# Optimization experiments

Hardware: AMD Instinct MI355X
Metric: run time of the kernel (lower is better)

The kernel has to match this reference:

```python
import jax, jax.numpy as jnp
import numpy as np

VOCAB = 780
HIDDEN = 256
DEPTH = 6
N_NODES = 65536
N_MESS = 131072
MAX_NEI = 5
N_TREES = 2048


def setup_inputs() -> dict:
    key = jax.random.key(0)
    ks = jax.random.split(key, 16)
    s = 0.05  # weight scale to avoid gate saturation
    return {
        "fnode": jax.random.randint(ks[0], (N_NODES,), 0, VOCAB),
        "fmess": jax.random.randint(ks[1], (N_MESS,), 0, N_NODES),
        "node_graph": jax.random.randint(ks[2], (N_NODES, MAX_NEI), 0, N_MESS),
        "mess_graph": jax.random.randint(ks[3], (N_MESS, MAX_NEI), 0, N_MESS),
        "scope_ids": jnp.sort(jax.random.randint(ks[4], (N_NODES,), 0, N_TREES)),
        "emb": jax.random.normal(ks[5], (VOCAB, HIDDEN), jnp.float32) * s,
        "Wz_w": jax.random.normal(ks[6], (2 * HIDDEN, HIDDEN), jnp.float32) * s,
        "Wz_b": jax.random.normal(ks[7], (HIDDEN,), jnp.float32) * s,
        "Wr_w": jax.random.normal(ks[8], (HIDDEN, HIDDEN), jnp.float32) * s,
        "Ur_w": jax.random.normal(ks[9], (HIDDEN, HIDDEN), jnp.float32) * s,
        "Ur_b": jax.random.normal(ks[10], (HIDDEN,), jnp.float32) * s,
        "Wh_w": jax.random.normal(ks[11], (2 * HIDDEN, HIDDEN), jnp.float32) * s,
        "Wh_b": jax.random.normal(ks[12], (HIDDEN,), jnp.float32) * s,
        "out_w": jax.random.normal(ks[13], (2 * HIDDEN, HIDDEN), jnp.float32) * s,
        "out_b": jax.random.normal(ks[14], (HIDDEN,), jnp.float32) * s,
    }


def reference(fnode, fmess, node_graph, mess_graph, scope_ids,
              emb, Wz_w, Wz_b, Wr_w, Ur_w, Ur_b, Wh_w, Wh_b, out_w, out_b):
    x_node = emb[fnode]            # [N, H] embedding lookup
    x = x_node[fmess]              # [M, H] source-node feature per message
    M = mess_graph.shape[0]
    mask = jnp.ones((M, 1), x.dtype).at[0].set(0.0)  # message 0 is padding
    r1 = x @ Wr_w                  # W_r(x), constant across depth (no bias)

    def gru_step(h, _):
        h_nei = h[mess_graph]                                  # [M, K, H] gather
        sum_h = h_nei.sum(axis=1)                              # [M, H]
        z = jax.nn.sigmoid(jnp.concatenate([x, sum_h], 1) @ Wz_w + Wz_b)
        r = jax.nn.sigmoid(r1[:, None, :] + h_nei @ Ur_w + Ur_b)  # [M, K, H]
        sum_gh = (r * h_nei).sum(axis=1)
        pre_h = jnp.tanh(jnp.concatenate([x, sum_gh], 1) @ Wh_w + Wh_b)
        h_new = ((1.0 - z) * sum_h + z * pre_h) * mask
        return h_new, None

    h0 = jnp.zeros((M, HIDDEN), x.dtype)
    h, _ = jax.lax.scan(gru_step, h0, None, length=DEPTH)

    mess_nei = h[node_graph].sum(axis=1)                       # [N, H]
    node_vec = jax.nn.relu(jnp.concatenate([x_node, mess_nei], 1) @ out_w + out_b)

    # per-tree mean over contiguous scopes (segment mean)
    sums = jax.ops.segment_sum(node_vec, scope_ids, num_segments=N_TREES)
    counts = jax.ops.segment_sum(jnp.ones((node_vec.shape[0],), node_vec.dtype),
                                 scope_ids, num_segments=N_TREES)
    return sums / jnp.maximum(counts, 1.0)[:, None]
```

## Files before the change

### kernel.cpp

```cpp
#include <hip/hip_runtime.h>


#define HD 256
#define NNODES 65536
#define NMESS 131072
#define NVOCAB 780
#define NTREES 2048
#define MAXNEI 5
#define BM 128
#define BMF 32
#define LDF 264

typedef short bfrag __attribute__((ext_vector_type(8)));
typedef short s16x8 __attribute__((ext_vector_type(8)));
typedef float f32x4v __attribute__((ext_vector_type(4)));
typedef float f32x2 __attribute__((ext_vector_type(2)));
typedef unsigned short ush;
typedef unsigned char u8;

__device__ __forceinline__ float bf2f(ush u) {
    union { unsigned int u; float f; } v; v.u = ((unsigned int)u) << 16; return v.f;
}
__device__ __forceinline__ float bfu_lo(unsigned int w) {
    union { unsigned int u; float f; } v; v.u = w << 16; return v.f;
}
__device__ __forceinline__ float bfu_hi(unsigned int w) {
    union { unsigned int u; float f; } v; v.u = w & 0xffff0000u; return v.f;
}
__device__ __forceinline__ ush f2bf_fast(float f) {
    union { float f; unsigned int u; } v; v.f = f;
    return (ush)((v.u + 0x8000u) >> 16);
}
__device__ __forceinline__ unsigned int pack2bf(float hi, float lo) {
    union { float f; unsigned int u; } a, b; a.f = hi; b.f = lo;
    return __builtin_amdgcn_perm(a.u + 0x8000u, b.u + 0x8000u, 0x07060302u);
}
__device__ __forceinline__ float sigm(float x) {
    return __builtin_amdgcn_rcpf(1.f + __expf(-x));
}
__device__ __forceinline__ float tanh_fast(float x) {
    return 1.f - 2.f * __builtin_amdgcn_rcpf(__expf(2.f * x) + 1.f);
}
__device__ __forceinline__ void async16(const ush* g, ush* l) {
    __builtin_amdgcn_global_load_lds(
        (const __attribute__((address_space(1))) unsigned int*)(g),
        (__attribute__((address_space(3))) unsigned int*)(l), 16, 0, 0);
}
__device__ __forceinline__ uint2 pack8fp8(const float* f) {
    int lo = __builtin_amdgcn_cvt_pk_fp8_f32(f[0], f[1], 0, 0);
    lo = __builtin_amdgcn_cvt_pk_fp8_f32(f[2], f[3], lo, 1);
    int hi = __builtin_amdgcn_cvt_pk_fp8_f32(f[4], f[5], 0, 0);
    hi = __builtin_amdgcn_cvt_pk_fp8_f32(f[6], f[7], hi, 1);
    uint2 o; o.x = (unsigned int)lo; o.y = (unsigned int)hi; return o;
}

__global__ __launch_bounds__(256) void prep_tables_sk(
    const float* __restrict__ emb,
    const float* __restrict__ Wz_w, const float* __restrict__ Wz_b,
    const float* __restrict__ Wr_w, const float* __restrict__ Ur_b,
    const float* __restrict__ Wh_w, const float* __restrict__ Wh_b,
    const float* __restrict__ out_w, const float* __restrict__ out_b,
    float* __restrict__ embR, float* __restrict__ embZ,
    float* __restrict__ embH, float* __restrict__ embO)
{
    __shared__ __align__(16) float e[4][64];
    int t = threadIdx.x;
    int b0 = blockIdx.x * 4;
    int k0 = blockIdx.y * 64;
    e[t >> 6][t & 63] = emb[(b0 + (t >> 6)) * HD + k0 + (t & 63)];
    __syncthreads();
    float aR[4] = {0,0,0,0}, aZ[4] = {0,0,0,0}, aH[4] = {0,0,0,0}, aO[4] = {0,0,0,0};
    for (int kk = 0; kk < 64; kk++) {
        int k = k0 + kk;
        float wr = Wr_w[k * HD + t];
        float wz = Wz_w[k * HD + t];
        float wh = Wh_w[k * HD + t];
        float wo = out_w[k * HD + t];
        #pragma unroll
        for (int r = 0; r < 4; r++) {
            float ev = e[r][kk];
            aR[r] += ev * wr; aZ[r] += ev * wz; aH[r] += ev * wh; aO[r] += ev * wo;
        }
    }
    if (blockIdx.y == 0) {
        float br = Ur_b[t], bz = Wz_b[t], bh = Wh_b[t], bo = out_b[t];
        #pragma unroll
        for (int r = 0; r < 4; r++) { aR[r] += br; aZ[r] += bz; aH[r] += bh; aO[r] += bo; }
    }
    #pragma unroll
    for (int r = 0; r < 4; r++) {
        atomicAdd(&embR[(b0 + r) * HD + t], aR[r]);
        atomicAdd(&embZ[(b0 + r) * HD + t], aZ[r]);
        atomicAdd(&embH[(b0 + r) * HD + t], aH[r]);
        atomicAdd(&embO[(b0 + r) * HD + t], aO[r]);
    }
}

__global__ __launch_bounds__(256) void h1fill(
    const float* __restrict__ embZ, const float* __restrict__ embH,
    ush* __restrict__ h1tab)
{
    int i = blockIdx.x * HD + threadIdx.x;
    h1tab[i] = f2bf_fast(sigm(embZ[i]) * tanh_fast(embH[i]));
}

__global__ __launch_bounds__(256) void h1u_sk(
    const ush* __restrict__ h1tab, const float* __restrict__ Ur_w,
    float* __restrict__ embU)
{
    __shared__ __align__(16) float e[4][64];
    int t = threadIdx.x;
    int b0 = blockIdx.x * 4;
    int k0 = blockIdx.y * 64;
    e[t >> 6][t & 63] = bf2f(h1tab[(b0 + (t >> 6)) * HD + k0 + (t & 63)]);
    __syncthreads();
    float aU[4] = {0,0,0,0};
    for (int kk = 0; kk < 64; kk++) {
        float w = Ur_w[(k0 + kk) * HD + t];
        #pragma unroll
        for (int r = 0; r < 4; r++) aU[r] += e[r][kk] * w;
    }
    #pragma unroll
    for (int r = 0; r < 4; r++) atomicAdd(&embU[(b0 + r) * HD + t], aU[r]);
}

__global__ __launch_bounds__(256) void prep_wt(
    const float* __restrict__ Ur_w, const float* __restrict__ Wz_w,
    const float* __restrict__ Wh_w, const float* __restrict__ out_w,
    ush* __restrict__ Wo2T,
    ush* __restrict__ Wz_p, ush* __restrict__ Wh_p, ush* __restrict__ Ur_p)
{
    int idx = blockIdx.x * 256 + threadIdx.x;
    int n = idx >> 8, k = idx & 255;
    Wo2T[idx] = f2bf_fast(out_w[(HD + k) * HD + n]);
    int paddr = ((((n >> 4) * 8 + (k >> 5)) * 64 + ((k >> 3) & 3) * 16 + (n & 15)) << 3) + (k & 7);
    Wz_p[paddr] = f2bf_fast(Wz_w[(HD + k) * HD + n]);
    Wh_p[paddr] = f2bf_fast(Wh_w[(HD + k) * HD + n]);
    Ur_p[paddr] = f2bf_fast(Ur_w[k * HD + n]);
}

__global__ __launch_bounds__(256) void prep_vmess(
    const int* __restrict__ fnode, const int* __restrict__ fmess,
    int* __restrict__ v_mess)
{
    int m = blockIdx.x * 256 + threadIdx.x;
    v_mess[m] = fnode[fmess[m]];
}

__global__ __launch_bounds__(256) void fill_h1(
    const ush* __restrict__ h1tab, const float* __restrict__ embU,
    const int* __restrict__ v_mess,
    ush* __restrict__ h, u8* __restrict__ hU8)
{
    int t = blockIdx.x * 256 + threadIdx.x;
    int m = t >> 5;
    int c = (t & 31) * 8;
    int v = v_mess[m];
    s16x8 o = *(const s16x8*)&h1tab[v * HD + c];
    float u[8];
    *(float4*)&u[0] = *(const float4*)&embU[v * HD + c];
    *(float4*)&u[4] = *(const float4*)&embU[v * HD + c + 4];
    uint2 up = pack8fp8(u);
    if (m == 0) { o = (s16x8){0,0,0,0,0,0,0,0}; up.x = up.y = 0; }
    *(s16x8*)&h[(size_t)m * HD + c] = o;
    *(uint2*)&hU8[(size_t)m * HD + c] = up;
}

__global__ __launch_bounds__(512) void gemm_out(
    const ush* __restrict__ A, const ush* __restrict__ Bt,
    float* __restrict__ C,
    const float* __restrict__ etab, const int* __restrict__ vids)
{
    __shared__ __align__(16) ush As[BM * 64];
    __shared__ __align__(16) ush Bs[HD * 64];
    int tid = threadIdx.x;
    int wave = tid >> 6, lane = tid & 63;
    int wm = wave >> 2, wn = wave & 3;
    int quad = lane >> 4, l16 = lane & 15;
    int row0 = blockIdx.x * BM;

    const ush* aG[2]; ush* aL[2];
    const ush* bG[4]; ush* bL[4];
    #pragma unroll
    for (int u = 0; u < 2; u++) {
        int cch = wave * 2 + u;
        int s = cch * 64 + lane;
        int r = s >> 3, p = s & 7, q = p ^ (r & 7);
        aG[u] = A + (size_t)(row0 + r) * HD + q * 8;
        aL[u] = &As[cch * 512];
    }
    #pragma unroll
    for (int u = 0; u < 4; u++) {
        int cch = wave * 4 + u;
        int s = cch * 64 + lane;
        int r = s >> 3, p = s & 7, q = p ^ (r & 7);
        bG[u] = Bt + (size_t)r * HD + q * 8;
        bL[u] = &Bs[cch * 512];
    }

    f32x4v acc[4][4] = {};

    for (int k0 = 0; k0 < HD; k0 += 64) {
        #pragma unroll
        for (int u = 0; u < 2; u++) async16(aG[u] + k0, aL[u]);
        #pragma unroll
        for (int u = 0; u < 4; u++) async16(bG[u] + k0, bL[u]);
        __syncthreads();
        #pragma unroll
        for (int ks = 0; ks < 64; ks += 32) {
            bfrag af[4], bff[4];
            #pragma unroll
            for (int i = 0; i < 4; i++) {
                int r = wm * 64 + i * 16 + l16;
                int q = (ks >> 3) + quad, p = q ^ (r & 7);
                af[i] = *(const bfrag*)&As[r * 64 + p * 8];
            }
            #pragma unroll
            for (int j = 0; j < 4; j++) {
                int r = wn * 64 + j * 16 + l16;
                int q = (ks >> 3) + quad, p = q ^ (r & 7);
                bff[j] = *(const bfrag*)&Bs[r * 64 + p * 8];
            }
            #pragma unroll
            for (int i = 0; i < 4; i++)
                #pragma unroll
                for (int j = 0; j < 4; j++)
                    acc[i][j] = __builtin_amdgcn_mfma_f32_16x16x32_bf16(af[i], bff[j], acc[i][j], 0, 0, 0);
        }
        __syncthreads();
    }
    #pragma unroll
    for (int i = 0; i < 4; i++) {
        #pragma unroll
        for (int j = 0; j < 4; j++) {
            int Cc = wn * 64 + j * 16 + l16;
            #pragma unroll
            for (int r = 0; r < 4; r++) {
                int Rr = row0 + wm * 64 + i * 16 + quad * 4 + r;
                float o = acc[i][j][r] + etab[vids[Rr] * HD + Cc];
                C[(size_t)Rr * HD + Cc] = fmaxf(o, 0.f);
            }
        }
    }
}

template<int EMIT_HU>
__global__ __launch_bounds__(256, 4) void fused_step(
    const ush* __restrict__ h, const u8* __restrict__ hU8,
    const int* __restrict__ mg, const int* __restrict__ v_mess,
    const float* __restrict__ embR, const float* __restrict__ embZ,
    const float* __restrict__ embH,
    const ush* __restrict__ Wz_p, const ush* __restrict__ Wh_p,
    const ush* __restrict__ Ur_p,
    ush* __restrict__ h_next, u8* __restrict__ hU8_next)
{
    __shared__ __align__(16) ush sh[BMF * LDF];
    __shared__ __align__(16) ush sg[BMF * LDF];
    int tid = threadIdx.x;
    int wv = tid >> 6, lane = tid & 63;
    int quad = lane >> 4, l16 = lane & 15;
    int m0 = blockIdx.x * BMF;

    #pragma unroll 2
    for (int it = 0; it < 4; it++) {
        int g = it * 256 + tid;
        int ml = g >> 5;
        int c = (g & 31) * 8;
        int m = m0 + ml;
        int v = v_mess[m];
        float rb[8];
        *(float4*)&rb[0] = *(const float4*)&embR[v * HD + c];
        *(float4*)&rb[4] = *(const float4*)&embR[v * HD + c + 4];
        float ah[8] = {0,0,0,0,0,0,0,0};
        float ag[8] = {0,0,0,0,0,0,0,0};
        #pragma unroll
        for (int kn = 0; kn < MAXNEI; kn++) {
            int j = mg[m * MAXNEI + kn];
            s16x8 hv = *(const s16x8*)&h[(size_t)j * HD + c];
            uint2 uv = *(const uint2*)&hU8[(size_t)j * HD + c];
            f32x2 u01 = __builtin_amdgcn_cvt_pk_f32_fp8((int)uv.x, false);
            f32x2 u23 = __builtin_amdgcn_cvt_pk_f32_fp8((int)uv.x, true);
            f32x2 u45 = __builtin_amdgcn_cvt_pk_f32_fp8((int)uv.y, false);
            f32x2 u67 = __builtin_amdgcn_cvt_pk_f32_fp8((int)uv.y, true);
            float uf[8] = {u01.x, u01.y, u23.x, u23.y, u45.x, u45.y, u67.x, u67.y};
            #pragma unroll
            for (int e = 0; e < 8; e++) {
                float hf = bf2f((ush)hv[e]);
                ah[e] += hf;
                ag[e] += sigm(rb[e] + uf[e]) * hf;
            }
        }
        uint4 oh, og;
        oh.x = pack2bf(ah[1], ah[0]); oh.y = pack2bf(ah[3], ah[2]);
        oh.z = pack2bf(ah[5], ah[4]); oh.w = pack2bf(ah[7], ah[6]);
        og.x = pack2bf(ag[1], ag[0]); og.y = pack2bf(ag[3], ag[2]);
        og.z = pack2bf(ag[5], ag[4]); og.w = pack2bf(ag[7], ag[6]);
        *(uint4*)&sh[ml * LDF + c] = oh;
        *(uint4*)&sg[ml * LDF + c] = og;
    }
    __syncthreads();

    f32x4v az[2][4] = {}, ap[2][4] = {};
    #pragma unroll
    for (int ksi = 0; ksi < 8; ksi++) {
        int ks = ksi * 32;
        bfrag ahf[2], agf[2], bz[4], bh[4];
        #pragma unroll
        for (int i = 0; i < 2; i++) {
            ahf[i] = *(const bfrag*)&sh[(i * 16 + l16) * LDF + ks + quad * 8];
            agf[i] = *(const bfrag*)&sg[(i * 16 + l16) * LDF + ks + quad * 8];
        }
        #pragma unroll
        for (int j = 0; j < 4; j++) {
            int f = ((wv * 4 + j) * 8 + ksi) * 64 + lane;
            bz[j] = *(const bfrag*)&Wz_p[(size_t)f * 8];
            bh[j] = *(const bfrag*)&Wh_p[(size_t)f * 8];
        }
        #pragma unroll
        for (int i = 0; i < 2; i++)
            #pragma unroll
            for (int j = 0; j < 4; j++) {
                az[i][j] = __builtin_amdgcn_mfma_f32_16x16x32_bf16(ahf[i], bz[j], az[i][j], 0, 0, 0);
                ap[i][j] = __builtin_amdgcn_mfma_f32_16x16x32_bf16(agf[i], bh[j], ap[i][j], 0, 0, 0);
            }
    }

    #pragma unroll
    for (int i = 0; i < 2; i++) {
        #pragma unroll
        for (int r = 0; r < 4; r++) {
            int rl = i * 16 + quad * 4 + r;
            int Rg = m0 + rl;
            int v = v_mess[Rg];
            #pragma unroll
            for (int j = 0; j < 4; j++) {
                int col = wv * 64 + j * 16 + l16;
                float z = sigm(az[i][j][r] + embZ[v * HD + col]);
                float pre = tanh_fast(ap[i][j][r] + embH[v * HD + col]);
                float shv = bf2f(sh[rl * LDF + col]);
                float hn = (1.f - z) * shv + z * pre;
                if (Rg == 0) hn = 0.f;
                az[i][j][r] = hn;
            }
        }
    }
    __syncthreads();

    #pragma unroll
    for (int i = 0; i < 2; i++)
        #pragma unroll
        for (int j = 0; j < 4; j++) {
            int col = wv * 64 + j * 16 + l16;
            #pragma unroll
            for (int r = 0; r < 4; r++)
                sg[(i * 16 + quad * 4 + r) * LDF + col] = f2bf_fast(az[i][j][r]);
        }
    __syncthreads();
    #pragma unroll
    for (int it = 0; it < 4; it++) {
        int g = it * 256 + tid;
        int ml = g >> 5;
        int c = (g & 31) * 8;
        *(uint4*)&h_next[(size_t)(m0 + ml) * HD + c] = *(const uint4*)&sg[ml * LDF + c];
    }

    if (EMIT_HU) {
        f32x4v au[2][4] = {};
        #pragma unroll
        for (int ksi = 0; ksi < 8; ksi++) {
            int ks = ksi * 32;
            bfrag af[2], bu[4];
            #pragma unroll
            for (int i = 0; i < 2; i++)
                af[i] = *(const bfrag*)&sg[(i * 16 + l16) * LDF + ks + quad * 8];
            #pragma unroll
            for (int j = 0; j < 4; j++) {
                int f = ((wv * 4 + j) * 8 + ksi) * 64 + lane;
                bu[j] = *(const bfrag*)&Ur_p[(size_t)f * 8];
            }
            #pragma unroll
            for (int i = 0; i < 2; i++)
                #pragma unroll
                for (int j = 0; j < 4; j++)
                    au[i][j] = __builtin_amdgcn_mfma_f32_16x16x32_bf16(af[i], bu[j], au[i][j], 0, 0, 0);
        }
        #pragma unroll
        for (int i = 0; i < 2; i++)
            #pragma unroll
            for (int j = 0; j < 4; j++) {
                int col = wv * 64 + j * 16 + l16;
                #pragma unroll
                for (int r = 0; r < 4; r++)
                    sh[(i * 16 + quad * 4 + r) * LDF + col] = f2bf_fast(au[i][j][r]);
            }
        __syncthreads();
        #pragma unroll
        for (int it = 0; it < 4; it++) {
            int g = it * 256 + tid;
            int ml = g >> 5;
            int c = (g & 31) * 8;
            uint4 w = *(const uint4*)&sh[ml * LDF + c];
            float f[8] = { bfu_lo(w.x), bfu_hi(w.x), bfu_lo(w.y), bfu_hi(w.y),
                           bfu_lo(w.z), bfu_hi(w.z), bfu_lo(w.w), bfu_hi(w.w) };
            uint2 o = pack8fp8(f);
            *(uint2*)&hU8_next[(size_t)(m0 + ml) * HD + c] = o;
        }
    }
}

__global__ __launch_bounds__(256) void gather_nodes(
    const ush* __restrict__ h, const int* __restrict__ ng,
    ush* __restrict__ mess_nei)
{
    int wave = threadIdx.x >> 6, lane = threadIdx.x & 63;
    int half = lane >> 5, li = lane & 31;
    int n = blockIdx.x * 8 + wave * 2 + half;
    int c = li * 8;
    float a[8] = {0,0,0,0,0,0,0,0};
    #pragma unroll
    for (int k = 0; k < MAXNEI; k++) {
        int j = ng[n * MAXNEI + k];
        s16x8 hv = *(const s16x8*)&h[(size_t)j * HD + c];
        #pragma unroll
        for (int e = 0; e < 8; e++) a[e] += bf2f((ush)hv[e]);
    }
    uint4 o;
    o.x = pack2bf(a[1], a[0]); o.y = pack2bf(a[3], a[2]);
    o.z = pack2bf(a[5], a[4]); o.w = pack2bf(a[7], a[6]);
    *(uint4*)&mess_nei[(size_t)n * HD + c] = o;
}

__device__ __forceinline__ int lower_bound_dev(const int* a, int n, int key) {
    int lo = 0, hi = n;
    while (lo < hi) { int mid = (lo + hi) >> 1; if (a[mid] < key) lo = mid + 1; else hi = mid; }
    return lo;
}

__global__ __launch_bounds__(256) void segment_mean(
    const float* __restrict__ node_vec, const int* __restrict__ scope,
    float* __restrict__ out)
{
    int t = blockIdx.x;
    int c = threadIdx.x;
    int lo = lower_bound_dev(scope, NNODES, t);
    int hi = lower_bound_dev(scope, NNODES, t + 1);
    float acc = 0.f;
    for (int n = lo; n < hi; n++) acc += node_vec[(size_t)n * HD + c];
    int cnt = hi - lo;
    out[t * HD + c] = cnt > 0 ? acc / (float)cnt : 0.f;
}

extern "C" void kernel_launch(void* const* d_in, const int* in_sizes, int n_in,
                              void* d_out, int out_size, void* d_ws, size_t ws_size,
                              hipStream_t stream)
{
    const int*   fnode      = (const int*)d_in[0];
    const int*   fmess      = (const int*)d_in[1];
    const int*   node_graph = (const int*)d_in[2];
    const int*   mess_graph = (const int*)d_in[3];
    const int*   scope_ids  = (const int*)d_in[4];
    const float* emb        = (const float*)d_in[5];
    const float* Wz_w       = (const float*)d_in[6];
    const float* Wz_b       = (const float*)d_in[7];
    const float* Wr_w       = (const float*)d_in[8];
    const float* Ur_w       = (const float*)d_in[9];
    const float* Ur_b       = (const float*)d_in[10];
    const float* Wh_w       = (const float*)d_in[11];
    const float* Wh_b       = (const float*)d_in[12];
    const float* out_w      = (const float*)d_in[13];
    const float* out_b      = (const float*)d_in[14];

    char* ws = (char*)d_ws;
    const size_t MHB = (size_t)NMESS * HD * 2;
    const size_t MH8 = (size_t)NMESS * HD;
    ush* P0 = (ush*)ws; ws += MHB;
    ush* P1 = (ush*)ws; ws += MHB;
    u8* U0 = (u8*)ws; ws += MH8;
    u8* U1 = (u8*)ws; ws += MH8;
    float* embR = (float*)ws; ws += (size_t)NVOCAB * HD * 4;
    float* embZ = (float*)ws; ws += (size_t)NVOCAB * HD * 4;
    float* embH = (float*)ws; ws += (size_t)NVOCAB * HD * 4;
    float* embO = (float*)ws; ws += (size_t)NVOCAB * HD * 4;
    float* embU = (float*)ws; ws += (size_t)NVOCAB * HD * 4;
    ush* h1tab = (ush*)ws; ws += (size_t)NVOCAB * HD * 2;
    ush* Wo2T  = (ush*)ws; ws += (size_t)HD * HD * 2;
    ush* Wz_p  = (ush*)ws; ws += (size_t)HD * HD * 2;
    ush* Wh_p  = (ush*)ws; ws += (size_t)HD * HD * 2;
    ush* Ur_p  = (ush*)ws; ws += (size_t)HD * HD * 2;
    int* v_mess = (int*)ws; ws += (size_t)NMESS * 4;
    if ((size_t)(ws - (char*)d_ws) > ws_size) return;

    hipMemsetAsync(embR, 0, (size_t)5 * NVOCAB * HD * 4, stream);
    prep_tables_sk<<<dim3(NVOCAB / 4, 4), 256, 0, stream>>>(
        emb, Wz_w, Wz_b, Wr_w, Ur_b, Wh_w, Wh_b, out_w, out_b,
        embR, embZ, embH, embO);
    h1fill<<<NVOCAB, 256, 0, stream>>>(embZ, embH, h1tab);
    h1u_sk<<<dim3(NVOCAB / 4, 4), 256, 0, stream>>>(h1tab, Ur_w, embU);
    prep_wt<<<HD * HD / 256, 256, 0, stream>>>(Ur_w, Wz_w, Wh_w, out_w,
                                               Wo2T, Wz_p, Wh_p, Ur_p);
    prep_vmess<<<NMESS / 256, 256, 0, stream>>>(fnode, fmess, v_mess);
    fill_h1<<<NMESS * 32 / 256, 256, 0, stream>>>(h1tab, embU, v_mess, P0, U0);

    ush* hc = P0; ush* hn = P1;
    u8* uc = U0; u8* un = U1;
    for (int d = 1; d < 5; d++) {
        fused_step<1><<<NMESS / BMF, 256, 0, stream>>>(hc, uc, mess_graph, v_mess,
                                                       embR, embZ, embH,
                                                       Wz_p, Wh_p, Ur_p, hn, un);
        { ush* t = hc; hc = hn; hn = t; }
        { u8* t = uc; uc = un; un = t; }
    }
    fused_step<0><<<NMESS / BMF, 256, 0, stream>>>(hc, uc, mess_graph, v_mess,
                                                   embR, embZ, embH,
                                                   Wz_p, Wh_p, Ur_p, hn, nullptr);
    hc = hn;

    ush* mess_nei = (ush*)U0;
    float* node_vec = (float*)(hc == P0 ? P1 : P0);
    gather_nodes<<<NNODES / 8, 256, 0, stream>>>(hc, node_graph, mess_nei);
    gemm_out<<<NNODES / BM, 512, 0, stream>>>(mess_nei, Wo2T, node_vec, embO, fnode);
    segment_mean<<<NTREES, 256, 0, stream>>>(node_vec, scope_ids, (float*)d_out);
}
```

Baseline: 1.087 ms.

## Fuse node neighbor gather with output GEMM using pre-packed weight fragments

Merges gather_nodes and gemm_out into one kernel, gather_out. Each block sums the neighbor message states for 32 nodes into shared memory, then runs MFMA against a fragment-packed out_w read directly from global memory, and applies the bias table and ReLU. This drops the bf16 mess_nei round trip through global memory and one kernel launch. In exchange the tiles are smaller and B fragments are no longer staged in LDS, so the weight is re-read from L2 by every block.

After: 1.077 ms. Within noise of the previous version (-0.9%).

```diff
diff --git a/kernel.cpp b/kernel.cpp
--- a/kernel.cpp
+++ b/kernel.cpp
@@ -7,7 +7,6 @@
 #define NVOCAB 780
 #define NTREES 2048
 #define MAXNEI 5
-#define BM 128
 #define BMF 32
 #define LDF 264
 
@@ -41,17 +40,20 @@
 __device__ __forceinline__ float tanh_fast(float x) {
     return 1.f - 2.f * __builtin_amdgcn_rcpf(__expf(2.f * x) + 1.f);
 }
-__device__ __forceinline__ void async16(const ush* g, ush* l) {
-    __builtin_amdgcn_global_load_lds(
-        (const __attribute__((address_space(1))) unsigned int*)(g),
-        (__attribute__((address_space(3))) unsigned int*)(l), 16, 0, 0);
-}
 __device__ __forceinline__ uint2 pack8fp8(const float* f) {
     int lo = __builtin_amdgcn_cvt_pk_fp8_f32(f[0], f[1], 0, 0);
     lo = __builtin_amdgcn_cvt_pk_fp8_f32(f[2], f[3], lo, 1);
     int hi = __builtin_amdgcn_cvt_pk_fp8_f32(f[4], f[5], 0, 0);
     hi = __builtin_amdgcn_cvt_pk_fp8_f32(f[6], f[7], hi, 1);
     uint2 o; o.x = (unsigned int)lo; o.y = (unsigned int)hi; return o;
+}
+__device__ __forceinline__ void fp8x8_to_f32(uint2 v, float* f) {
+    f32x2 a = __builtin_amdgcn_cvt_pk_f32_fp8((int)v.x, false);
+    f32x2 b = __builtin_amdgcn_cvt_pk_f32_fp8((int)v.x, true);
+    f32x2 c = __builtin_amdgcn_cvt_pk_f32_fp8((int)v.y, false);
+    f32x2 d = __builtin_amdgcn_cvt_pk_f32_fp8((int)v.y, true);
+    f[0] = a.x; f[1] = a.y; f[2] = b.x; f[3] = b.y;
+    f[4] = c.x; f[5] = c.y; f[6] = d.x; f[7] = d.y;
 }
 
 __global__ __launch_bounds__(256) void prep_tables_sk(
@@ -127,13 +129,13 @@
 __global__ __launch_bounds__(256) void prep_wt(
     const float* __restrict__ Ur_w, const float* __restrict__ Wz_w,
     const float* __restrict__ Wh_w, const float* __restrict__ out_w,
-    ush* __restrict__ Wo2T,
+    ush* __restrict__ Wo_p,
     ush* __restrict__ Wz_p, ush* __restrict__ Wh_p, ush* __restrict__ Ur_p)
 {
     int idx = blockIdx.x * 256 + threadIdx.x;
     int n = idx >> 8, k = idx & 255;
-    Wo2T[idx] = f2bf_fast(out_w[(HD + k) * HD + n]);
     int paddr = ((((n >> 4) * 8 + (k >> 5)) * 64 + ((k >> 3) & 3) * 16 + (n & 15)) << 3) + (k & 7);
+    Wo_p[paddr] = f2bf_fast(out_w[(HD + k) * HD + n]);
     Wz_p[paddr] = f2bf_fast(Wz_w[(HD + k) * HD + n]);
     Wh_p[paddr] = f2bf_fast(Wh_w[(HD + k) * HD + n]);
     Ur_p[paddr] = f2bf_fast(Ur_w[k * HD + n]);
@@ -166,84 +168,6 @@
     *(uint2*)&hU8[(size_t)m * HD + c] = up;
 }
 
-__global__ __launch_bounds__(512) void gemm_out(
-    const ush* __restrict__ A, const ush* __restrict__ Bt,
-    float* __restrict__ C,
-    const float* __restrict__ etab, const int* __restrict__ vids)
-{
-    __shared__ __align__(16) ush As[BM * 64];
-    __shared__ __align__(16) ush Bs[HD * 64];
-    int tid = threadIdx.x;
-    int wave = tid >> 6, lane = tid & 63;
-    int wm = wave >> 2, wn = wave & 3;
-    int quad = lane >> 4, l16 = lane & 15;
-    int row0 = blockIdx.x * BM;
-
-    const ush* aG[2]; ush* aL[2];
-    const ush* bG[4]; ush* bL[4];
-    #pragma unroll
-    for (int u = 0; u < 2; u++) {
-        int cch = wave * 2 + u;
-        int s = cch * 64 + lane;
-        int r = s >> 3, p = s & 7, q = p ^ (r & 7);
-        aG[u] = A + (size_t)(row0 + r) * HD + q * 8;
-        aL[u] = &As[cch * 512];
-    }
-    #pragma unroll
-    for (int u = 0; u < 4; u++) {
-        int cch = wave * 4 + u;
-        int s = cch * 64 + lane;
-        int r = s >> 3, p = s & 7, q = p ^ (r & 7);
-        bG[u] = Bt + (size_t)r * HD + q * 8;
-        bL[u] = &Bs[cch * 512];
-    }
-
-    f32x4v acc[4][4] = {};
-
-    for (int k0 = 0; k0 < HD; k0 += 64) {
-        #pragma unroll
-        for (int u = 0; u < 2; u++) async16(aG[u] + k0, aL[u]);
-        #pragma unroll
-        for (int u = 0; u < 4; u++) async16(bG[u] + k0, bL[u]);
-        __syncthreads();
-        #pragma unroll
-        for (int ks = 0; ks < 64; ks += 32) {
-            bfrag af[4], bff[4];
-            #pragma unroll
-            for (int i = 0; i < 4; i++) {
-                int r = wm * 64 + i * 16 + l16;
-                int q = (ks >> 3) + quad, p = q ^ (r & 7);
-                af[i] = *(const bfrag*)&As[r * 64 + p * 8];
-            }
-            #pragma unroll
-            for (int j = 0; j < 4; j++) {
-                int r = wn * 64 + j * 16 + l16;
-                int q = (ks >> 3) + quad, p = q ^ (r & 7);
-                bff[j] = *(const bfrag*)&Bs[r * 64 + p * 8];
-            }
-            #pragma unroll
-            for (int i = 0; i < 4; i++)
-                #pragma unroll
-                for (int j = 0; j < 4; j++)
-                    acc[i][j] = __builtin_amdgcn_mfma_f32_16x16x32_bf16(af[i], bff[j], acc[i][j], 0, 0, 0);
-        }
-        __syncthreads();
-    }
-    #pragma unroll
-    for (int i = 0; i < 4; i++) {
-        #pragma unroll
-        for (int j = 0; j < 4; j++) {
-            int Cc = wn * 64 + j * 16 + l16;
-            #pragma unroll
-            for (int r = 0; r < 4; r++) {
-                int Rr = row0 + wm * 64 + i * 16 + quad * 4 + r;
-                float o = acc[i][j][r] + etab[vids[Rr] * HD + Cc];
-                C[(size_t)Rr * HD + Cc] = fmaxf(o, 0.f);
-            }
-        }
-    }
-}
-
 template<int EMIT_HU>
 __global__ __launch_bounds__(256, 4) void fused_step(
     const ush* __restrict__ h, const u8* __restrict__ hU8,
@@ -277,12 +201,9 @@
         for (int kn = 0; kn < MAXNEI; kn++) {
             int j = mg[m * MAXNEI + kn];
             s16x8 hv = *(const s16x8*)&h[(size_t)j * HD + c];
-            uint2 uv = *(const uint2*)&hU8[(size_t)j * HD + c];
-            f32x2 u01 = __builtin_amdgcn_cvt_pk_f32_fp8((int)uv.x, false);
-            f32x2 u23 = __builtin_amdgcn_cvt_pk_f32_fp8((int)uv.x, true);
-            f32x2 u45 = __builtin_amdgcn_cvt_pk_f32_fp8((int)uv.y, false);
-            f32x2 u67 = __builtin_amdgcn_cvt_pk_f32_fp8((int)uv.y, true);
-            float uf[8] = {u01.x, u01.y, u23.x, u23.y, u45.x, u45.y, u67.x, u67.y};
+            uint2 uv8 = *(const uint2*)&hU8[(size_t)j * HD + c];
+            float uf[8];
+            fp8x8_to_f32(uv8, uf);
             #pragma unroll
             for (int e = 0; e < 8; e++) {
                 float hf = bf2f((ush)hv[e]);
@@ -408,26 +329,72 @@
     }
 }
 
-__global__ __launch_bounds__(256) void gather_nodes(
+__global__ __launch_bounds__(256) void gather_out(
     const ush* __restrict__ h, const int* __restrict__ ng,
-    ush* __restrict__ mess_nei)
-{
-    int wave = threadIdx.x >> 6, lane = threadIdx.x & 63;
-    int half = lane >> 5, li = lane & 31;
-    int n = blockIdx.x * 8 + wave * 2 + half;
-    int c = li * 8;
-    float a[8] = {0,0,0,0,0,0,0,0};
-    #pragma unroll
-    for (int k = 0; k < MAXNEI; k++) {
-        int j = ng[n * MAXNEI + k];
-        s16x8 hv = *(const s16x8*)&h[(size_t)j * HD + c];
-        #pragma unroll
-        for (int e = 0; e < 8; e++) a[e] += bf2f((ush)hv[e]);
-    }
-    uint4 o;
-    o.x = pack2bf(a[1], a[0]); o.y = pack2bf(a[3], a[2]);
-    o.z = pack2bf(a[5], a[4]); o.w = pack2bf(a[7], a[6]);
-    *(uint4*)&mess_nei[(size_t)n * HD + c] = o;
+    const int* __restrict__ fnode, const float* __restrict__ embO,
+    const ush* __restrict__ Wo_p, float* __restrict__ node_vec)
+{
+    __shared__ __align__(16) ush sh[BMF * LDF];
+    int tid = threadIdx.x;
+    int wv = tid >> 6, lane = tid & 63;
+    int quad = lane >> 4, l16 = lane & 15;
+    int n0 = blockIdx.x * BMF;
+
+    #pragma unroll 2
+    for (int it = 0; it < 4; it++) {
+        int g = it * 256 + tid;
+        int ml = g >> 5;
+        int c = (g & 31) * 8;
+        int n = n0 + ml;
+        float a[8] = {0,0,0,0,0,0,0,0};
+        #pragma unroll
+        for (int kn = 0; kn < MAXNEI; kn++) {
+            int j = ng[n * MAXNEI + kn];
+            s16x8 hv = *(const s16x8*)&h[(size_t)j * HD + c];
+            #pragma unroll
+            for (int e = 0; e < 8; e++) a[e] += bf2f((ush)hv[e]);
+        }
+        uint4 o;
+        o.x = pack2bf(a[1], a[0]); o.y = pack2bf(a[3], a[2]);
+        o.z = pack2bf(a[5], a[4]); o.w = pack2bf(a[7], a[6]);
+        *(uint4*)&sh[ml * LDF + c] = o;
+    }
+    __syncthreads();
+
+    f32x4v acc[2][4] = {};
+    #pragma unroll
+    for (int ksi = 0; ksi < 8; ksi++) {
+        int ks = ksi * 32;
+        bfrag af[2], bo[4];
+        #pragma unroll
+        for (int i = 0; i < 2; i++)
+            af[i] = *(const bfrag*)&sh[(i * 16 + l16) * LDF + ks + quad * 8];
+        #pragma unroll
+        for (int j = 0; j < 4; j++) {
+            int f = ((wv * 4 + j) * 8 + ksi) * 64 + lane;
+            bo[j] = *(const bfrag*)&Wo_p[(size_t)f * 8];
+        }
+        #pragma unroll
+        for (int i = 0; i < 2; i++)
+            #pragma unroll
+            for (int j = 0; j < 4; j++)
+                acc[i][j] = __builtin_amdgcn_mfma_f32_16x16x32_bf16(af[i], bo[j], acc[i][j], 0, 0, 0);
+    }
+
+    #pragma unroll
+    for (int i = 0; i < 2; i++) {
+        #pragma unroll
+        for (int r = 0; r < 4; r++) {
+            int Rn = n0 + i * 16 + quad * 4 + r;
+            int v = fnode[Rn];
+            #pragma unroll
+            for (int j = 0; j < 4; j++) {
+                int col = wv * 64 + j * 16 + l16;
+                float o = acc[i][j][r] + embO[v * HD + col];
+                node_vec[(size_t)Rn * HD + col] = fmaxf(o, 0.f);
+            }
+        }
+    }
 }
 
 __device__ __forceinline__ int lower_bound_dev(const int* a, int n, int key) {
@@ -483,11 +450,12 @@
     float* embO = (float*)ws; ws += (size_t)NVOCAB * HD * 4;
     float* embU = (float*)ws; ws += (size_t)NVOCAB * HD * 4;
     ush* h1tab = (ush*)ws; ws += (size_t)NVOCAB * HD * 2;
-    ush* Wo2T  = (ush*)ws; ws += (size_t)HD * HD * 2;
+    ush* Wo_p  = (ush*)ws; ws += (size_t)HD * HD * 2;
     ush* Wz_p  = (ush*)ws; ws += (size_t)HD * HD * 2;
     ush* Wh_p  = (ush*)ws; ws += (size_t)HD * HD * 2;
     ush* Ur_p  = (ush*)ws; ws += (size_t)HD * HD * 2;
     int* v_mess = (int*)ws; ws += (size_t)NMESS * 4;
+    float* node_vec = (float*)U0;
     if ((size_t)(ws - (char*)d_ws) > ws_size) return;
 
     hipMemsetAsync(embR, 0, (size_t)5 * NVOCAB * HD * 4, stream);
@@ -497,7 +465,7 @@
     h1fill<<<NVOCAB, 256, 0, stream>>>(embZ, embH, h1tab);
     h1u_sk<<<dim3(NVOCAB / 4, 4), 256, 0, stream>>>(h1tab, Ur_w, embU);
     prep_wt<<<HD * HD / 256, 256, 0, stream>>>(Ur_w, Wz_w, Wh_w, out_w,
-                                               Wo2T, Wz_p, Wh_p, Ur_p);
+                                               Wo_p, Wz_p, Wh_p, Ur_p);
     prep_vmess<<<NMESS / 256, 256, 0, stream>>>(fnode, fmess, v_mess);
     fill_h1<<<NMESS * 32 / 256, 256, 0, stream>>>(h1tab, embU, v_mess, P0, U0);
 
@@ -515,9 +483,7 @@
                                                    Wz_p, Wh_p, Ur_p, hn, nullptr);
     hc = hn;
 
-    ush* mess_nei = (ush*)U0;
-    float* node_vec = (float*)(hc == P0 ? P1 : P0);
-    gather_nodes<<<NNODES / 8, 256, 0, stream>>>(hc, node_graph, mess_nei);
-    gemm_out<<<NNODES / BM, 512, 0, stream>>>(mess_nei, Wo2T, node_vec, embO, fnode);
+    gather_out<<<NNODES / BMF, 256, 0, stream>>>(hc, node_graph, fnode, embO,
+                                                 Wo_p, node_vec);
     segment_mean<<<NTREES, 256, 0, stream>>>(node_vec, scope_ids, (float*)d_out);
 }
```
